# Performance work log

Measured on AMD Instinct MI355X. Metric: run time of the kernel, lower is better.

## Reference

```python
import jax, jax.numpy as jnp
import numpy as np
import math

TILE_SIZE = 32
N_HEADS = 16
FACTOR = 5.0
MASK_VALUE = -1e9


def setup_inputs() -> dict:
    key = jax.random.key(0)
    ks = jax.random.split(key, 8)
    B, S, D = 2, 2048, 1024
    w = 0.02  # weight scale so attention logits stay in a sane range
    return {
        "query": jax.random.normal(ks[0], (B, S, D), jnp.float32),
        "key": jax.random.normal(ks[1], (B, S, D), jnp.float32),
        "value": jax.random.normal(ks[2], (B, S, D), jnp.float32),
        "mask": jnp.zeros((1, 1, S, S), jnp.float32),
        "Wq": jax.random.normal(ks[3], (D, D), jnp.float32) * w,
        "bq": jnp.zeros((D,), jnp.float32),
        "Wk": jax.random.normal(ks[4], (D, D), jnp.float32) * w,
        "bk": jnp.zeros((D,), jnp.float32),
        "Wv": jax.random.normal(ks[5], (D, D), jnp.float32) * w,
        "bv": jnp.zeros((D,), jnp.float32),
        "Wo": jax.random.normal(ks[6], (D, D), jnp.float32) * w,
        "bo": jnp.zeros((D,), jnp.float32),
        "q_valid_len": 2000,
        "k_valid_len": 1900,
    }


def _pad_to_multiple(x, multiple):
    L = x.shape[1]
    p = (-L) % multiple  # static
    if p:
        x = jnp.pad(x, ((0, 0), (0, p), (0, 0)))
    return x, L


def _split_heads(x, H):
    B, L, D = x.shape
    return x.reshape(B, L, H, D // H).transpose(0, 2, 1, 3)  # [B,H,L,hd]


def _forward(query, key, value, mask, Wq, bq, Wk, bk, Wv, bv, Wo, bo,
             q_valid_len, k_valid_len):
    B, Sq, D = query.shape
    H = N_HEADS
    hd = D // H
    q = query @ Wq.T + bq
    k = key @ Wk.T + bk
    v = value @ Wv.T + bv
    q, q_len_pad = _pad_to_multiple(q, TILE_SIZE)
    k, _ = _pad_to_multiple(k, TILE_SIZE)
    v, _ = _pad_to_multiple(v, TILE_SIZE)
    qh, kh, vh = _split_heads(q, H), _split_heads(k, H), _split_heads(v, H)
    Lq, Lk = qh.shape[2], kh.shape[2]

    # key padding mask [1,1,1,Lk]
    kpm = ((jnp.arange(Lk) >= k_valid_len).astype(jnp.float32) * MASK_VALUE)
    attn_mask = mask + kpm.reshape(1, 1, 1, Lk)

    # manual scaled-dot attention with bf16 cast of scores (stable softmax path)
    scores = jnp.einsum('bhqd,bhkd->bhqk', qh, kh) / math.sqrt(hd)
    scores = scores.astype(jnp.bfloat16) + attn_mask.astype(jnp.bfloat16)
    probs = jax.nn.softmax(scores, axis=-1).astype(vh.dtype)
    context = jnp.einsum('bhqk,bhkd->bhqd', probs, vh)

    # ProbSparse top-u query-selection mask (note: original passes q_len_pad,
    # the pre-padding length, as valid_length)
    u = max(1, int(FACTOR * math.log(max(2, q_valid_len))))
    q_norm = jnp.sum(qh * qh, axis=-1)  # [B,H,Lq]
    if q_len_pad < Lq:
        q_norm = jnp.where(jnp.arange(Lq) < q_len_pad, q_norm, MASK_VALUE)
    _, topk_idx = jax.lax.top_k(q_norm, u)  # [B,H,u]
    # scatter ones at top-u positions (indices unique -> one-hot sum == set)
    ps_mask = jnp.sum(jax.nn.one_hot(topk_idx, Lq, dtype=jnp.float32), axis=2)
    context = context * ps_mask[..., None]

    # merge heads, strip padding, output projection (dropout p=0 / eval)
    context = context.transpose(0, 2, 1, 3).reshape(B, Lq, D)[:, :Sq, :]
    return context @ Wo.T + bo


def reference(query, key, value, mask, Wq, bq, Wk, bk, Wv, bv, Wo, bo,
              q_valid_len, k_valid_len):
    return _forward(query, key, value, mask, Wq, bq, Wk, bk, Wv, bv, Wo, bo,
                    q_valid_len, k_valid_len)
```

## Files before the change

kernel.cpp:

```cpp
#include <hip/hip_runtime.h>

typedef unsigned short u16;
typedef __bf16 bf16x8 __attribute__((ext_vector_type(8)));
typedef float f32x4 __attribute__((ext_vector_type(4)));

__device__ __forceinline__ u16 f2bf(float f){
  unsigned int x = __float_as_uint(f);
  unsigned int r = (x + 0x7FFFu + ((x >> 16) & 1u)) >> 16;
  return (u16)r;
}
__device__ __forceinline__ float bf2f(u16 u){
  return __uint_as_float(((unsigned int)u) << 16);
}
__device__ __forceinline__ int compute_u(int qvlv){
  int mm = qvlv > 2 ? qvlv : 2;
  int u = (int)(5.0 * log((double)mm));
  if (u < 1) u = 1;
  if (u > 64) u = 64;
  return u;
}
__device__ __forceinline__ void gload_lds16(const void* g, void* l){
  __builtin_amdgcn_global_load_lds(
      (const __attribute__((address_space(1))) void*)g,
      (__attribute__((address_space(3))) void*)l, 16, 0, 0);
}

__global__ void expand_kernel(const float* __restrict__ xq, const float* __restrict__ xk,
                              const float* __restrict__ xv,
                              const float* __restrict__ wq, const float* __restrict__ wk,
                              const float* __restrict__ wv,
                              u16* __restrict__ X1, u16* __restrict__ X2,
                              u16* __restrict__ W1, u16* __restrict__ W2)
{
  size_t g = (size_t)blockIdx.x * 256 + threadIdx.x;
  const float* src; u16 *d1, *d2;
  if (g < 3145728ull) {
    int p = (int)(g >> 20);
    size_t e = (g & 1048575ull) * 4;
    src = (p == 0 ? xq : (p == 1 ? xk : xv)) + e;
    size_t o = (size_t)p * 4194304ull + e;
    d1 = X1 + o; d2 = X2 + o;
  } else {
    size_t wg = g - 3145728ull;
    int p = (int)(wg >> 18);
    size_t e = (wg & 262143ull) * 4;
    src = (p == 0 ? wq : (p == 1 ? wk : wv)) + e;
    size_t o = (size_t)p * 1048576ull + e;
    d1 = W1 + o; d2 = W2 + o;
  }
  float4 x = *reinterpret_cast<const float4*>(src);
  float xs[4] = {x.x, x.y, x.z, x.w};
  u16 h1[4], h2[4];
#pragma unroll
  for (int i = 0; i < 4; ++i){
    float v = xs[i];
    u16 a = f2bf(v);  float r1 = v - bf2f(a);
    h1[i] = a; h2[i] = f2bf(r1);
  }
  *reinterpret_cast<ushort4*>(d1) = make_ushort4(h1[0], h1[1], h1[2], h1[3]);
  *reinterpret_cast<ushort4*>(d2) = make_ushort4(h2[0], h2[1], h2[2], h2[3]);
}

__global__ void wot_kernel(const float* __restrict__ Wo, float* __restrict__ WoT){
  __shared__ float tile[32][33];
  int tx = threadIdx.x, ty = threadIdx.y;
  int bx = blockIdx.x * 32, by = blockIdx.y * 32;
#pragma unroll
  for (int r = 0; r < 4; ++r)
    tile[ty + r*8][tx] = Wo[(size_t)(by + ty + r*8) * 1024 + bx + tx];
  __syncthreads();
#pragma unroll
  for (int r = 0; r < 4; ++r)
    WoT[(size_t)(bx + ty + r*8) * 1024 + by + tx] = tile[tx][ty + r*8];
}

__global__ __launch_bounds__(512, 1) void gemm_proj(
    const u16* __restrict__ X1, const u16* __restrict__ X2,
    const u16* __restrict__ W1, const u16* __restrict__ W2,
    const float* __restrict__ bq, const float* __restrict__ bk, const float* __restrict__ bv,
    float* __restrict__ PROJ)
{
  int z = blockIdx.z;
  int orig = blockIdx.x + blockIdx.y * 8;
  int wgid = (orig & 7) * 16 + (orig >> 3);
  int bx = wgid & 7, by = wgid >> 3;

  const u16* Xa0 = X1 + (size_t)z * 4194304;
  const u16* Xa1 = X2 + (size_t)z * 4194304;
  const u16* Wb0 = W1 + (size_t)z * 1048576;
  const u16* Wb1 = W2 + (size_t)z * 1048576;
  const float* bias = (z == 0) ? bq : (z == 1 ? bk : bv);
  float* C = PROJ + (size_t)z * 4194304;

  __shared__ __align__(16) u16 T[2 * 24576];
  u16* SET0 = T;
  u16* SET1 = T + 24576;

  int t = threadIdx.x;
  int wave = t >> 6, lane = t & 63;
  int wm = wave >> 1, wn = wave & 1;
  int lr = lane & 15, lk = lane >> 4;
  int rowA = by * 256, rowB = bx * 128;
  f32x4 acc[4][4] = {};
  bf16x8 afA[4], afB[4], bgA[4], bgB[4];

#define STAGEA(dstbase, G)                                                    \
  {                                                                           \
    _Pragma("unroll")                                                         \
    for (int i = 0; i < 2; ++i){                                              \
      int p = i * 512 + t;                                                    \
      int r = p >> 2;                                                         \
      int c = (p & 3) ^ ((r >> 1) & 3);                                       \
      gload_lds16(G + (size_t)(rowA + r) * 1024 + pk + c * 8,                 \
                  (dstbase) + p * 8);                                         \
    }                                                                         \
  }
#define STAGEB(dstbase, G)                                                    \
  {                                                                           \
    int p = t;                                                                \
    int r = p >> 2;                                                           \
    int c = (p & 3) ^ ((r >> 1) & 3);                                         \
    gload_lds16(G + (size_t)(rowB + r) * 1024 + pk + c * 8,                   \
                (dstbase) + p * 8);                                           \
  }
#define STAGE_SET(S)                                                          \
  {                                                                           \
    STAGEA((S), Xa0); STAGEA((S) + 8192, Xa1);                                \
    STAGEB((S) + 16384, Wb0); STAGEB((S) + 20480, Wb1);                       \
  }
#define LOADA(dst, tile)                                                      \
  {                                                                           \
    _Pragma("unroll")                                                         \
    for (int m = 0; m < 4; ++m){                                              \
      int r = wm * 64 + m * 16 + lr;                                          \
      dst[m] = *reinterpret_cast<const bf16x8*>(                              \
          &(tile)[r * 32 + ((lk ^ ((r >> 1) & 3)) << 3)]);                    \
    }                                                                         \
  }
#define LOADB(dst, tile)                                                      \
  {                                                                           \
    _Pragma("unroll")                                                         \
    for (int n = 0; n < 4; ++n){                                              \
      int r = wn * 64 + n * 16 + lr;                                          \
      dst[n] = *reinterpret_cast<const bf16x8*>(                              \
          &(tile)[r * 32 + ((lk ^ ((r >> 1) & 3)) << 3)]);                    \
    }                                                                         \
  }
#define GRPX(A_, B_)                                                          \
  {                                                                           \
    __builtin_amdgcn_s_setprio(1);                                            \
    _Pragma("unroll")                                                         \
    for (int m = 0; m < 4; ++m)                                               \
      _Pragma("unroll")                                                       \
      for (int n = 0; n < 4; ++n)                                             \
        acc[m][n] = __builtin_amdgcn_mfma_f32_16x16x32_bf16(A_[m], B_[n],     \
                                                            acc[m][n], 0,0,0);\
    __builtin_amdgcn_s_setprio(0);                                            \
  }

  {
    int pk = 0;
    STAGE_SET(SET0);
  }
  __syncthreads();

  for (int kt = 0; kt < 32; ++kt){
    u16* CUR = (kt & 1) ? SET1 : SET0;
    u16* NXT = (kt & 1) ? SET0 : SET1;
    if (kt < 31){
      int pk = (kt + 1) * 32;
      STAGE_SET(NXT);
    }
    __builtin_amdgcn_sched_barrier(0);
    u16* A0t = CUR;          u16* A1t = CUR + 8192;
    u16* B0t = CUR + 16384;  u16* B1t = CUR + 20480;
    LOADA(afA, A0t); LOADB(bgA, B0t);
    LOADB(bgB, B1t); GRPX(afA, bgA);
    LOADA(afB, A1t); GRPX(afA, bgB);
                     GRPX(afB, bgA);
    __syncthreads();
  }
#undef STAGEA
#undef STAGEB
#undef STAGE_SET
#undef LOADA
#undef LOADB
#undef GRPX

  if (z == 0){
#pragma unroll
    for (int m = 0; m < 4; ++m){
      int row0 = by * 256 + wm * 64 + m * 16 + lk * 4;
#pragma unroll
      for (int n = 0; n < 4; ++n){
        int col = bx * 128 + wn * 64 + n * 16 + lr;
        float bb = bias[col];
#pragma unroll
        for (int j = 0; j < 4; ++j)
          C[(size_t)(row0 + j) * 1024 + col] = acc[m][n][j] + bb;
      }
    }
  } else if (z == 1){
    u16* KS = (u16*)C;
#pragma unroll
    for (int m = 0; m < 4; ++m){
      int r0 = by * 256 + wm * 64 + m * 16 + lk * 4;
      int b = r0 >> 11, kb = r0 & 2047;
#pragma unroll
      for (int n = 0; n < 4; ++n){
        int c = bx * 128 + wn * 64 + n * 16 + lr;
        float bb = bias[c];
        int h = c >> 6, d = c & 63;
#pragma unroll
        for (int j = 0; j < 4; ++j){
          float v = acc[m][n][j] + bb;
          u16 hi = f2bf(v);
          u16 lo = f2bf(v - bf2f(hi));
          size_t base = ((size_t)(b * 16 + h) * 2048 + (size_t)(kb + j)) * 128;
          KS[base + d] = hi;
          KS[base + 64 + d] = lo;
        }
      }
    }
  } else {
    u16* VT = (u16*)C;
#pragma unroll
    for (int m = 0; m < 4; ++m){
      int r0 = by * 256 + wm * 64 + m * 16 + lk * 4;
      int b = r0 >> 11, kb = r0 & 2047;
#pragma unroll
      for (int n = 0; n < 4; ++n){
        int c = bx * 128 + wn * 64 + n * 16 + lr;
        float bb = bias[c];
        int h = c >> 6, d = c & 63;
        u16 hi[4], lo[4];
#pragma unroll
        for (int j = 0; j < 4; ++j){
          float v = acc[m][n][j] + bb;
          hi[j] = f2bf(v);
          lo[j] = f2bf(v - bf2f(hi[j]));
        }
        size_t base = ((size_t)(b * 16 + h) * 128) * 2048 + (size_t)kb;
        *reinterpret_cast<ushort4*>(&VT[base + (size_t)d * 2048]) =
            make_ushort4(hi[0], hi[1], hi[2], hi[3]);
        *reinterpret_cast<ushort4*>(&VT[base + (size_t)(64 + d) * 2048]) =
            make_ushort4(lo[0], lo[1], lo[2], lo[3]);
      }
    }
  }
}

__global__ __launch_bounds__(256) void qnorm_kernel(const float* __restrict__ PROJ,
                                                    float* __restrict__ qn,
                                                    unsigned int* __restrict__ hmask){
  int t = threadIdx.x;
  int gid = blockIdx.x * 256 + t;
  if (gid < 4096) hmask[gid] = 0;
  int h = t >> 4, q4 = t & 15;
#pragma unroll
  for (int it = 0; it < 8; ++it){
    int tok = blockIdx.x * 8 + it;
    const float* row = PROJ + (size_t)tok * 1024;
    float4 x = *reinterpret_cast<const float4*>(&row[h * 64 + q4 * 4]);
    float s = x.x*x.x + x.y*x.y + x.z*x.z + x.w*x.w;
    s += __shfl_xor(s, 1);
    s += __shfl_xor(s, 2);
    s += __shfl_xor(s, 4);
    s += __shfl_xor(s, 8);
    if (q4 == 0){
      int b = tok >> 11, l = tok & 2047;
      qn[(size_t)(b * 16 + h) * 2048 + l] = s;
    }
  }
}

__global__ __launch_bounds__(512) void topk_kernel(
    const float* __restrict__ qn, int* __restrict__ topk,
    unsigned char* __restrict__ seli, unsigned int* __restrict__ hmask,
    const int* __restrict__ qvlp){
  int bh = blockIdx.x; int b = bh >> 4, h = bh & 15;
  int u = compute_u(qvlp[0]);
  int t = threadIdx.x;
  float4 v4 = *reinterpret_cast<const float4*>(qn + (size_t)bh * 2048 + t * 4);
  float v[4] = {v4.x, v4.y, v4.z, v4.w};
  __shared__ float swv[8];
  __shared__ int swi[8];
  __shared__ int sidx;
  int lane = t & 63, w = t >> 6;
  for (int it = 0; it < u; ++it){
    float bv = v[0]; int bi = t * 4;
#pragma unroll
    for (int j = 1; j < 4; ++j){
      if (v[j] > bv){ bv = v[j]; bi = t * 4 + j; }
    }
#pragma unroll
    for (int off = 1; off < 64; off <<= 1){
      float ov = __shfl_xor(bv, off);
      int   oi = __shfl_xor(bi, off);
      if (ov > bv || (ov == bv && oi < bi)){ bv = ov; bi = oi; }
    }
    if (lane == 0){ swv[w] = bv; swi[w] = bi; }
    __syncthreads();
    if (t == 0){
      float fv = swv[0]; int fi = swi[0];
#pragma unroll
      for (int k = 1; k < 8; ++k){
        if (swv[k] > fv || (swv[k] == fv && swi[k] < fi)){ fv = swv[k]; fi = swi[k]; }
      }
      sidx = fi;
      topk[bh * 64 + it] = fi;
      seli[(size_t)bh * 2048 + fi] = (unsigned char)it;
      atomicOr(&hmask[b * 2048 + fi], 1u << h);
    }
    __syncthreads();
    int idx = sidx;
    if ((idx >> 2) == t) v[idx & 3] = -3.4e38f;
  }
}

__global__ void qs_gather(const float* __restrict__ PROJ, const int* __restrict__ topk,
                          u16* __restrict__ QS, const int* __restrict__ qvlp){
  int bh = blockIdx.x; int b = bh >> 4, h = bh & 15;
  int u = compute_u(qvlp[0]);
  __shared__ int idx[64];
  int t = threadIdx.x;
  if (t < 64) idx[t] = (t < u) ? topk[bh * 64 + t] : 0;
  __syncthreads();
  for (int e = t; e < 64 * 64; e += 256){
    int i = e >> 6, d = e & 63;
    float v = 0.f;
    if (i < u) v = PROJ[(size_t)(b * 2048 + idx[i]) * 1024 + h * 64 + d];
    u16 hi = f2bf(v);
    u16 lo = f2bf(v - bf2f(hi));
    QS[(size_t)bh * 8192 + i * 128 + d] = hi;
    QS[(size_t)bh * 8192 + i * 128 + 64 + d] = lo;
  }
}

__global__ __launch_bounds__(256) void scores_mfma(
    const u16* __restrict__ QS, const u16* __restrict__ KS,
    const int* __restrict__ topk, const float* __restrict__ maskp,
    u16* __restrict__ sc, const int* __restrict__ qvlp, const int* __restrict__ kvlp)
{
  int bh = blockIdx.y;
  int kvlv = kvlp[0]; if (kvlv > 2048) kvlv = 2048; if (kvlv < 0) kvlv = 0;
  int u = compute_u(qvlp[0]);
  int k0 = blockIdx.x * 128;
  if (k0 >= kvlv) return;
  int t = threadIdx.x, wave = t >> 6, lane = t & 63;
  int lr = lane & 15, lk = lane >> 4;
  __shared__ int idx_l[64];
  if (t < 64) idx_l[t] = (t < u) ? topk[bh * 64 + t] : 0;
  __syncthreads();
  const u16* Qb = QS + (size_t)bh * 8192;
  const u16* Kb = KS + (size_t)bh * 2048 * 128;
  bf16x8 ah[2], al[2];
#pragma unroll
  for (int ks = 0; ks < 2; ++ks){
    const u16* qrow = &Qb[(wave * 16 + lr) * 128];
    ah[ks] = *reinterpret_cast<const bf16x8*>(&qrow[ks * 32 + lk * 8]);
    al[ks] = *reinterpret_cast<const bf16x8*>(&qrow[64 + ks * 32 + lk * 8]);
  }
  f32x4 acc[8] = {};
#pragma unroll
  for (int n = 0; n < 8; ++n){
    const u16* krow = &Kb[(size_t)(k0 + n * 16 + lr) * 128];
    bf16x8 bh0 = *reinterpret_cast<const bf16x8*>(&krow[lk * 8]);
    bf16x8 bh1 = *reinterpret_cast<const bf16x8*>(&krow[32 + lk * 8]);
    bf16x8 bl0 = *reinterpret_cast<const bf16x8*>(&krow[64 + lk * 8]);
    bf16x8 bl1 = *reinterpret_cast<const bf16x8*>(&krow[96 + lk * 8]);
    acc[n] = __builtin_amdgcn_mfma_f32_16x16x32_bf16(ah[0], bh0, acc[n], 0, 0, 0);
    acc[n] = __builtin_amdgcn_mfma_f32_16x16x32_bf16(ah[0], bl0, acc[n], 0, 0, 0);
    acc[n] = __builtin_amdgcn_mfma_f32_16x16x32_bf16(al[0], bh0, acc[n], 0, 0, 0);
    acc[n] = __builtin_amdgcn_mfma_f32_16x16x32_bf16(al[0], bl0, acc[n], 0, 0, 0);
    acc[n] = __builtin_amdgcn_mfma_f32_16x16x32_bf16(ah[1], bh1, acc[n], 0, 0, 0);
    acc[n] = __builtin_amdgcn_mfma_f32_16x16x32_bf16(ah[1], bl1, acc[n], 0, 0, 0);
    acc[n] = __builtin_amdgcn_mfma_f32_16x16x32_bf16(al[1], bh1, acc[n], 0, 0, 0);
    acc[n] = __builtin_amdgcn_mfma_f32_16x16x32_bf16(al[1], bl1, acc[n], 0, 0, 0);
  }
#pragma unroll
  for (int n = 0; n < 8; ++n){
    int k = k0 + n * 16 + lr;
    if (k >= kvlv) continue;
#pragma unroll
    for (int j = 0; j < 4; ++j){
      int i = wave * 16 + lk * 4 + j;
      if (i >= u) continue;
      float s = acc[n][j] * 0.125f;
      u16 xb = f2bf(s);
      u16 mb = f2bf(maskp[(size_t)idx_l[i] * 2048 + k]);
      u16 xm = f2bf(bf2f(xb) + bf2f(mb));
      sc[(size_t)(bh * 64 + i) * 2048 + k] = xm;
    }
  }
}

__global__ void softmax_kernel(u16* __restrict__ sc, const int* __restrict__ qvlp,
                               const int* __restrict__ kvlp){
  int bh = blockIdx.y, i = blockIdx.x;
  int u = compute_u(qvlp[0]);
  if (i >= u) return;
  int kvlv = kvlp[0]; if (kvlv > 2048) kvlv = 2048; if (kvlv < 0) kvlv = 0;
  u16* row = sc + (size_t)(bh * 64 + i) * 2048;
  int t = threadIdx.x;
  float x[8];
  float lm = -3.4e38f;
#pragma unroll
  for (int j = 0; j < 8; ++j){
    int k = t + j * 256;
    x[j] = (k < kvlv) ? bf2f(row[k]) : -3.4e38f;
    lm = fmaxf(lm, x[j]);
  }
  __shared__ float red[256];
  red[t] = lm; __syncthreads();
  for (int s = 128; s > 0; s >>= 1){ if (t < s) red[t] = fmaxf(red[t], red[t+s]); __syncthreads(); }
  float m = red[0];
  __syncthreads();
  float e[8]; float ls = 0.f;
#pragma unroll
  for (int j = 0; j < 8; ++j){
    int k = t + j * 256;
    if (k < kvlv){
      u16 ub = f2bf(x[j] - m);
      u16 eb = f2bf(expf(bf2f(ub)));
      e[j] = bf2f(eb);
      ls += e[j];
    } else e[j] = 0.f;
  }
  red[t] = ls; __syncthreads();
  for (int s = 128; s > 0; s >>= 1){ if (t < s) red[t] += red[t+s]; __syncthreads(); }
  float S = red[0];
  float Sb = bf2f(f2bf(S));
#pragma unroll
  for (int j = 0; j < 8; ++j){
    int k = t + j * 256;
    if (k < 2048) row[k] = (k < kvlv) ? f2bf(e[j] / Sb) : (u16)0;
  }
}

__global__ void pv_mfma(const u16* __restrict__ probs, const u16* __restrict__ VT,
                        float* __restrict__ part, const int* __restrict__ kvlp)
{
  int bh = blockIdx.y; int b = bh >> 4, h = bh & 15;
  int kvlv = kvlp[0]; if (kvlv > 2048) kvlv = 2048; if (kvlv < 0) kvlv = 0;
  int kc = blockIdx.x;
  int k0 = kc * 128;
  if (k0 >= kvlv) return;
  int t = threadIdx.x, w = t >> 6, lane = t & 63;
  int lr = lane & 15, lk = lane >> 4;
  const u16* Pb = probs + (size_t)bh * 64 * 2048;
  const u16* Vb = VT + (size_t)(b * 16 + h) * 128 * 2048;
  f32x4 acc[4] = {};
#pragma unroll
  for (int ks = 0; ks < 4; ++ks){
    int kk = k0 + ks * 32 + lk * 8;
    bf16x8 A0 = *reinterpret_cast<const bf16x8*>(Pb + (size_t)(lr     ) * 2048 + kk);
    bf16x8 A1 = *reinterpret_cast<const bf16x8*>(Pb + (size_t)(lr + 16) * 2048 + kk);
    bf16x8 A2 = *reinterpret_cast<const bf16x8*>(Pb + (size_t)(lr + 32) * 2048 + kk);
    bf16x8 A3 = *reinterpret_cast<const bf16x8*>(Pb + (size_t)(lr + 48) * 2048 + kk);
    bf16x8 Bh = *reinterpret_cast<const bf16x8*>(Vb + (size_t)(w * 16 + lr     ) * 2048 + kk);
    bf16x8 Bl = *reinterpret_cast<const bf16x8*>(Vb + (size_t)(w * 16 + lr + 64) * 2048 + kk);
    acc[0] = __builtin_amdgcn_mfma_f32_16x16x32_bf16(A0, Bh, acc[0], 0, 0, 0);
    acc[1] = __builtin_amdgcn_mfma_f32_16x16x32_bf16(A1, Bh, acc[1], 0, 0, 0);
    acc[2] = __builtin_amdgcn_mfma_f32_16x16x32_bf16(A2, Bh, acc[2], 0, 0, 0);
    acc[3] = __builtin_amdgcn_mfma_f32_16x16x32_bf16(A3, Bh, acc[3], 0, 0, 0);
    acc[0] = __builtin_amdgcn_mfma_f32_16x16x32_bf16(A0, Bl, acc[0], 0, 0, 0);
    acc[1] = __builtin_amdgcn_mfma_f32_16x16x32_bf16(A1, Bl, acc[1], 0, 0, 0);
    acc[2] = __builtin_amdgcn_mfma_f32_16x16x32_bf16(A2, Bl, acc[2], 0, 0, 0);
    acc[3] = __builtin_amdgcn_mfma_f32_16x16x32_bf16(A3, Bl, acc[3], 0, 0, 0);
  }
  float* pc = part + (size_t)(kc * 32 + bh) * 64 * 64;
#pragma unroll
  for (int m = 0; m < 4; ++m){
    int row = m * 16 + lk * 4;
#pragma unroll
    for (int j = 0; j < 4; ++j)
      pc[(size_t)(row + j) * 64 + w * 16 + lr] = acc[m][j];
  }
}

__global__ void pv_reduce(const float* __restrict__ part, float* __restrict__ ctx,
                          const int* __restrict__ qvlp, const int* __restrict__ kvlp){
  int bh = blockIdx.y, r = blockIdx.x;
  int u = compute_u(qvlp[0]);
  if (r >= u) return;
  int kvlv = kvlp[0]; if (kvlv > 2048) kvlv = 2048; if (kvlv < 0) kvlv = 0;
  int kcmax = (kvlv + 127) / 128;
  int d = threadIdx.x;
  float s = 0.f;
  for (int kc = 0; kc < kcmax; ++kc)
    s += part[(size_t)((kc * 32 + bh) * 64 + r) * 64 + d];
  ctx[(size_t)(bh * 64 + r) * 64 + d] = s;
}

__global__ void outproj_kernel(const float* __restrict__ ctx, const float* __restrict__ WoT,
                               const float* __restrict__ bo, const unsigned int* __restrict__ hmask,
                               const unsigned char* __restrict__ seli, float* __restrict__ out){
  int row = blockIdx.x;
  int b = row >> 11, l = row & 2047;
  int t = threadIdx.x;
  float acc[4];
#pragma unroll
  for (int r = 0; r < 4; ++r) acc[r] = bo[t + r * 256];
  unsigned int m = hmask[row];
  __shared__ float clds[64];
  while (m){
    int h = __ffs(m) - 1; m &= (m - 1);
    int i = (int)seli[(size_t)(b * 16 + h) * 2048 + l];
    __syncthreads();
    if (t < 64) clds[t] = ctx[(size_t)((b * 16 + h) * 64 + i) * 64 + t];
    __syncthreads();
    for (int j = 0; j < 64; ++j){
      float c = clds[j];
      const float* wrow = &WoT[(size_t)(h * 64 + j) * 1024];
#pragma unroll
      for (int r = 0; r < 4; ++r) acc[r] += c * wrow[t + r * 256];
    }
  }
  float* orow = out + (size_t)row * 1024;
#pragma unroll
  for (int r = 0; r < 4; ++r) orow[t + r * 256] = acc[r];
}

__global__ void fail_fill(float* o, int n){
  int i = blockIdx.x * 256 + threadIdx.x;
  if (i < n) o[i] = 12345.0f;
}

extern "C" void kernel_launch(void* const* d_in, const int* in_sizes, int n_in,
                              void* d_out, int out_size, void* d_ws, size_t ws_size,
                              hipStream_t stream)
{
  const float* query = (const float*)d_in[0];
  const float* key   = (const float*)d_in[1];
  const float* value = (const float*)d_in[2];
  const float* maskp = (const float*)d_in[3];
  const float* Wq = (const float*)d_in[4];
  const float* bq = (const float*)d_in[5];
  const float* Wk = (const float*)d_in[6];
  const float* bk = (const float*)d_in[7];
  const float* Wv = (const float*)d_in[8];
  const float* bv = (const float*)d_in[9];
  const float* Wo = (const float*)d_in[10];
  const float* bo = (const float*)d_in[11];
  const int* qvl = (const int*)d_in[12];
  const int* kvl = (const int*)d_in[13];
  float* out = (float*)d_out;

  char* ws = (char*)d_ws;
  size_t off = 0;
  auto alloc = [&](size_t bytes) -> void* {
    void* p = ws + off;
    off = (off + bytes + 255) & ~(size_t)255;
    return p;
  };
  u16* X1 = (u16*)alloc(3ull * 4194304 * 2);
  u16* X2 = (u16*)alloc(3ull * 4194304 * 2);
  u16* W1 = (u16*)alloc(3ull * 1048576 * 2);
  u16* W2 = (u16*)alloc(3ull * 1048576 * 2);
  float* PROJ = (float*)alloc(3ull * 4194304 * 4);
  float* WOT  = (float*)alloc(4194304ull);
  float* QN   = (float*)alloc(2ull * 16 * 2048 * 4);
  int*   TOPK = (int*)alloc(2ull * 16 * 64 * 4);
  unsigned char* SELI = (unsigned char*)alloc(2ull * 16 * 2048);
  unsigned int* HMASK = (unsigned int*)alloc(2ull * 2048 * 4);
  u16*   SC   = (u16*)alloc(2048ull * 2048 * 2);
  float* CTX  = (float*)alloc(2048ull * 64 * 4);
  u16*   QS   = (u16*)alloc(32ull * 64 * 128 * 2);

  u16* KS = (u16*)(PROJ + 1ull * 4194304);
  u16* VT = (u16*)(PROJ + 2ull * 4194304);
  float* PART = (float*)X1;

  if (ws_size < off){
    fail_fill<<<(out_size + 255) / 256, 256, 0, stream>>>(out, out_size);
    return;
  }

  expand_kernel<<<15360, 256, 0, stream>>>(query, key, value, Wq, Wk, Wv,
                                           X1, X2, W1, W2);
  wot_kernel<<<dim3(32, 32), dim3(32, 8), 0, stream>>>(Wo, WOT);
  gemm_proj<<<dim3(8, 16, 3), 512, 0, stream>>>(X1, X2, W1, W2, bq, bk, bv, PROJ);
  qnorm_kernel<<<512, 256, 0, stream>>>(PROJ, QN, HMASK);
  topk_kernel<<<32, 512, 0, stream>>>(QN, TOPK, SELI, HMASK, qvl);
  qs_gather<<<32, 256, 0, stream>>>(PROJ, TOPK, QS, qvl);
  scores_mfma<<<dim3(16, 32), 256, 0, stream>>>(QS, KS, TOPK, maskp, SC, qvl, kvl);
  softmax_kernel<<<dim3(64, 32), 256, 0, stream>>>(SC, qvl, kvl);
  pv_mfma<<<dim3(16, 32), 256, 0, stream>>>(SC, VT, PART, kvl);
  pv_reduce<<<dim3(64, 32), 64, 0, stream>>>(PART, CTX, qvl, kvl);
  outproj_kernel<<<4096, 256, 0, stream>>>(CTX, WOT, bo, HMASK, SELI, out);
}
```

Measured before the change: 259.3 us.

## Fuse small kernels: WoT into expand, qnorm into GEMM epilogue, topk+gather, reduce into outproj

Merges the Wo transpose and hmask clearing into the expand kernel. Computes per-head query norms in the Q-projection GEMM epilogue using shuffles instead of rereading PROJ. Replaces the block-wide top-k with a single-wavefront register top-k fused with the QS gather, and folds the partial-sum reduction into the output projection. The goal is to cut kernel launches and global round trips. The cost is a serial single-wave top-k and redundant partial reductions for each selected row in outproj.

```diff
diff --git a/kernel.cpp b/kernel.cpp
--- a/kernel.cpp
+++ b/kernel.cpp
@@ -30,9 +30,27 @@
                               const float* __restrict__ wq, const float* __restrict__ wk,
                               const float* __restrict__ wv,
                               u16* __restrict__ X1, u16* __restrict__ X2,
-                              u16* __restrict__ W1, u16* __restrict__ W2)
+                              u16* __restrict__ W1, u16* __restrict__ W2,
+                              const float* __restrict__ Wo, float* __restrict__ WoT,
+                              unsigned int* __restrict__ hmask)
 {
-  size_t g = (size_t)blockIdx.x * 256 + threadIdx.x;
+  __shared__ float tile[32][33];
+  int t = threadIdx.x;
+  if (blockIdx.x >= 15360){
+    int bid = blockIdx.x - 15360;
+    int bx = (bid & 31) * 32, by = (bid >> 5) * 32;
+    int tx = t & 31, ty = t >> 5;
+#pragma unroll
+    for (int r = 0; r < 4; ++r)
+      tile[ty + r*8][tx] = Wo[(size_t)(by + ty + r*8) * 1024 + bx + tx];
+    __syncthreads();
+#pragma unroll
+    for (int r = 0; r < 4; ++r)
+      WoT[(size_t)(bx + ty + r*8) * 1024 + by + tx] = tile[tx][ty + r*8];
+    return;
+  }
+  size_t g = (size_t)blockIdx.x * 256 + t;
+  if (g < 4096) hmask[g] = 0;
   const float* src; u16 *d1, *d2;
   if (g < 3145728ull) {
     int p = (int)(g >> 20);
@@ -61,24 +79,11 @@
   *reinterpret_cast<ushort4*>(d2) = make_ushort4(h2[0], h2[1], h2[2], h2[3]);
 }
 
-__global__ void wot_kernel(const float* __restrict__ Wo, float* __restrict__ WoT){
-  __shared__ float tile[32][33];
-  int tx = threadIdx.x, ty = threadIdx.y;
-  int bx = blockIdx.x * 32, by = blockIdx.y * 32;
-#pragma unroll
-  for (int r = 0; r < 4; ++r)
-    tile[ty + r*8][tx] = Wo[(size_t)(by + ty + r*8) * 1024 + bx + tx];
-  __syncthreads();
-#pragma unroll
-  for (int r = 0; r < 4; ++r)
-    WoT[(size_t)(bx + ty + r*8) * 1024 + by + tx] = tile[tx][ty + r*8];
-}
-
 __global__ __launch_bounds__(512, 1) void gemm_proj(
     const u16* __restrict__ X1, const u16* __restrict__ X2,
     const u16* __restrict__ W1, const u16* __restrict__ W2,
     const float* __restrict__ bq, const float* __restrict__ bk, const float* __restrict__ bv,
-    float* __restrict__ PROJ)
+    float* __restrict__ PROJ, float* __restrict__ qn)
 {
   int z = blockIdx.z;
   int orig = blockIdx.x + blockIdx.y * 8;
@@ -188,6 +193,7 @@
 #undef GRPX
 
   if (z == 0){
+    float sq[4][4] = {};
 #pragma unroll
     for (int m = 0; m < 4; ++m){
       int row0 = by * 256 + wm * 64 + m * 16 + lk * 4;
@@ -196,8 +202,27 @@
         int col = bx * 128 + wn * 64 + n * 16 + lr;
         float bb = bias[col];
 #pragma unroll
-        for (int j = 0; j < 4; ++j)
-          C[(size_t)(row0 + j) * 1024 + col] = acc[m][n][j] + bb;
+        for (int j = 0; j < 4; ++j){
+          float v = acc[m][n][j] + bb;
+          C[(size_t)(row0 + j) * 1024 + col] = v;
+          sq[m][j] += v * v;
+        }
+      }
+    }
+    int hh = bx * 2 + wn;
+#pragma unroll
+    for (int m = 0; m < 4; ++m){
+#pragma unroll
+      for (int j = 0; j < 4; ++j){
+        float s = sq[m][j];
+        s += __shfl_xor(s, 1);
+        s += __shfl_xor(s, 2);
+        s += __shfl_xor(s, 4);
+        s += __shfl_xor(s, 8);
+        if (lr == 0){
+          int row = by * 256 + wm * 64 + m * 16 + lk * 4 + j;
+          qn[(size_t)((row >> 11) * 16 + hh) * 2048 + (row & 2047)] = s;
+        }
       }
     }
   } else if (z == 1){
@@ -250,86 +275,48 @@
   }
 }
 
-__global__ __launch_bounds__(256) void qnorm_kernel(const float* __restrict__ PROJ,
-                                                    float* __restrict__ qn,
-                                                    unsigned int* __restrict__ hmask){
-  int t = threadIdx.x;
-  int gid = blockIdx.x * 256 + t;
-  if (gid < 4096) hmask[gid] = 0;
-  int h = t >> 4, q4 = t & 15;
-#pragma unroll
-  for (int it = 0; it < 8; ++it){
-    int tok = blockIdx.x * 8 + it;
-    const float* row = PROJ + (size_t)tok * 1024;
-    float4 x = *reinterpret_cast<const float4*>(&row[h * 64 + q4 * 4]);
-    float s = x.x*x.x + x.y*x.y + x.z*x.z + x.w*x.w;
-    s += __shfl_xor(s, 1);
-    s += __shfl_xor(s, 2);
-    s += __shfl_xor(s, 4);
-    s += __shfl_xor(s, 8);
-    if (q4 == 0){
-      int b = tok >> 11, l = tok & 2047;
-      qn[(size_t)(b * 16 + h) * 2048 + l] = s;
-    }
-  }
-}
-
-__global__ __launch_bounds__(512) void topk_kernel(
+__global__ __launch_bounds__(256) void topk_kernel(
     const float* __restrict__ qn, int* __restrict__ topk,
     unsigned char* __restrict__ seli, unsigned int* __restrict__ hmask,
+    const float* __restrict__ PROJ, u16* __restrict__ QS,
     const int* __restrict__ qvlp){
   int bh = blockIdx.x; int b = bh >> 4, h = bh & 15;
   int u = compute_u(qvlp[0]);
   int t = threadIdx.x;
-  float4 v4 = *reinterpret_cast<const float4*>(qn + (size_t)bh * 2048 + t * 4);
-  float v[4] = {v4.x, v4.y, v4.z, v4.w};
-  __shared__ float swv[8];
-  __shared__ int swi[8];
-  __shared__ int sidx;
-  int lane = t & 63, w = t >> 6;
-  for (int it = 0; it < u; ++it){
-    float bv = v[0]; int bi = t * 4;
-#pragma unroll
-    for (int j = 1; j < 4; ++j){
-      if (v[j] > bv){ bv = v[j]; bi = t * 4 + j; }
-    }
-#pragma unroll
-    for (int off = 1; off < 64; off <<= 1){
-      float ov = __shfl_xor(bv, off);
-      int   oi = __shfl_xor(bi, off);
-      if (ov > bv || (ov == bv && oi < bi)){ bv = ov; bi = oi; }
-    }
-    if (lane == 0){ swv[w] = bv; swi[w] = bi; }
-    __syncthreads();
-    if (t == 0){
-      float fv = swv[0]; int fi = swi[0];
-#pragma unroll
-      for (int k = 1; k < 8; ++k){
-        if (swv[k] > fv || (swv[k] == fv && swi[k] < fi)){ fv = swv[k]; fi = swi[k]; }
-      }
-      sidx = fi;
-      topk[bh * 64 + it] = fi;
-      seli[(size_t)bh * 2048 + fi] = (unsigned char)it;
-      atomicOr(&hmask[b * 2048 + fi], 1u << h);
-    }
-    __syncthreads();
-    int idx = sidx;
-    if ((idx >> 2) == t) v[idx & 3] = -3.4e38f;
-  }
-}
-
-__global__ void qs_gather(const float* __restrict__ PROJ, const int* __restrict__ topk,
-                          u16* __restrict__ QS, const int* __restrict__ qvlp){
-  int bh = blockIdx.x; int b = bh >> 4, h = bh & 15;
-  int u = compute_u(qvlp[0]);
-  __shared__ int idx[64];
-  int t = threadIdx.x;
-  if (t < 64) idx[t] = (t < u) ? topk[bh * 64 + t] : 0;
+  __shared__ int sidx_l[64];
+  if (t < 64){
+    int lane = t;
+    float v[32];
+#pragma unroll
+    for (int j = 0; j < 32; ++j) v[j] = qn[(size_t)bh * 2048 + j * 64 + lane];
+    for (int it = 0; it < u; ++it){
+      float bv = v[0]; int bi = lane;
+#pragma unroll
+      for (int j = 1; j < 32; ++j){
+        if (v[j] > bv){ bv = v[j]; bi = j * 64 + lane; }
+      }
+#pragma unroll
+      for (int off = 1; off < 64; off <<= 1){
+        float ov = __shfl_xor(bv, off);
+        int   oi = __shfl_xor(bi, off);
+        if (ov > bv || (ov == bv && oi < bi)){ bv = ov; bi = oi; }
+      }
+      if (lane == 0){
+        topk[bh * 64 + it] = bi;
+        seli[(size_t)bh * 2048 + bi] = (unsigned char)it;
+        atomicOr(&hmask[b * 2048 + bi], 1u << h);
+        sidx_l[it] = bi;
+      }
+#pragma unroll
+      for (int j = 0; j < 32; ++j)
+        if (j * 64 + lane == bi) v[j] = -3.4e38f;
+    }
+  }
   __syncthreads();
   for (int e = t; e < 64 * 64; e += 256){
     int i = e >> 6, d = e & 63;
     float v = 0.f;
-    if (i < u) v = PROJ[(size_t)(b * 2048 + idx[i]) * 1024 + h * 64 + d];
+    if (i < u) v = PROJ[(size_t)(b * 2048 + sidx_l[i]) * 1024 + h * 64 + d];
     u16 hi = f2bf(v);
     u16 lo = f2bf(v - bf2f(hi));
     QS[(size_t)bh * 8192 + i * 128 + d] = hi;
@@ -479,26 +466,15 @@
   }
 }
 
-__global__ void pv_reduce(const float* __restrict__ part, float* __restrict__ ctx,
-                          const int* __restrict__ qvlp, const int* __restrict__ kvlp){
-  int bh = blockIdx.y, r = blockIdx.x;
-  int u = compute_u(qvlp[0]);
-  if (r >= u) return;
-  int kvlv = kvlp[0]; if (kvlv > 2048) kvlv = 2048; if (kvlv < 0) kvlv = 0;
-  int kcmax = (kvlv + 127) / 128;
-  int d = threadIdx.x;
-  float s = 0.f;
-  for (int kc = 0; kc < kcmax; ++kc)
-    s += part[(size_t)((kc * 32 + bh) * 64 + r) * 64 + d];
-  ctx[(size_t)(bh * 64 + r) * 64 + d] = s;
-}
-
-__global__ void outproj_kernel(const float* __restrict__ ctx, const float* __restrict__ WoT,
+__global__ void outproj_kernel(const float* __restrict__ part, const float* __restrict__ WoT,
                                const float* __restrict__ bo, const unsigned int* __restrict__ hmask,
-                               const unsigned char* __restrict__ seli, float* __restrict__ out){
+                               const unsigned char* __restrict__ seli, float* __restrict__ out,
+                               const int* __restrict__ kvlp){
   int row = blockIdx.x;
   int b = row >> 11, l = row & 2047;
   int t = threadIdx.x;
+  int kvlv = kvlp[0]; if (kvlv > 2048) kvlv = 2048; if (kvlv < 0) kvlv = 0;
+  int kcmax = (kvlv + 127) / 128;
   float acc[4];
 #pragma unroll
   for (int r = 0; r < 4; ++r) acc[r] = bo[t + r * 256];
@@ -506,9 +482,15 @@
   __shared__ float clds[64];
   while (m){
     int h = __ffs(m) - 1; m &= (m - 1);
-    int i = (int)seli[(size_t)(b * 16 + h) * 2048 + l];
+    int bh = b * 16 + h;
+    int i = (int)seli[(size_t)bh * 2048 + l];
     __syncthreads();
-    if (t < 64) clds[t] = ctx[(size_t)((b * 16 + h) * 64 + i) * 64 + t];
+    if (t < 64){
+      float s = 0.f;
+      for (int kc = 0; kc < kcmax; ++kc)
+        s += part[(size_t)((kc * 32 + bh) * 64 + i) * 64 + t];
+      clds[t] = s;
+    }
     __syncthreads();
     for (int j = 0; j < 64; ++j){
       float c = clds[j];
@@ -565,7 +547,6 @@
   unsigned char* SELI = (unsigned char*)alloc(2ull * 16 * 2048);
   unsigned int* HMASK = (unsigned int*)alloc(2ull * 2048 * 4);
   u16*   SC   = (u16*)alloc(2048ull * 2048 * 2);
-  float* CTX  = (float*)alloc(2048ull * 64 * 4);
   u16*   QS   = (u16*)alloc(32ull * 64 * 128 * 2);
 
   u16* KS = (u16*)(PROJ + 1ull * 4194304);
@@ -577,16 +558,12 @@
     return;
   }
 
-  expand_kernel<<<15360, 256, 0, stream>>>(query, key, value, Wq, Wk, Wv,
-                                           X1, X2, W1, W2);
-  wot_kernel<<<dim3(32, 32), dim3(32, 8), 0, stream>>>(Wo, WOT);
-  gemm_proj<<<dim3(8, 16, 3), 512, 0, stream>>>(X1, X2, W1, W2, bq, bk, bv, PROJ);
-  qnorm_kernel<<<512, 256, 0, stream>>>(PROJ, QN, HMASK);
-  topk_kernel<<<32, 512, 0, stream>>>(QN, TOPK, SELI, HMASK, qvl);
-  qs_gather<<<32, 256, 0, stream>>>(PROJ, TOPK, QS, qvl);
+  expand_kernel<<<16384, 256, 0, stream>>>(query, key, value, Wq, Wk, Wv,
+                                           X1, X2, W1, W2, Wo, WOT, HMASK);
+  gemm_proj<<<dim3(8, 16, 3), 512, 0, stream>>>(X1, X2, W1, W2, bq, bk, bv, PROJ, QN);
+  topk_kernel<<<32, 256, 0, stream>>>(QN, TOPK, SELI, HMASK, PROJ, QS, qvl);
   scores_mfma<<<dim3(16, 32), 256, 0, stream>>>(QS, KS, TOPK, maskp, SC, qvl, kvl);
   softmax_kernel<<<dim3(64, 32), 256, 0, stream>>>(SC, qvl, kvl);
   pv_mfma<<<dim3(16, 32), 256, 0, stream>>>(SC, VT, PART, kvl);
-  pv_reduce<<<dim3(64, 32), 64, 0, stream>>>(PART, CTX, qvl, kvl);
-  outproj_kernel<<<4096, 256, 0, stream>>>(CTX, WOT, bo, HMASK, SELI, out);
-}
+  outproj_kernel<<<4096, 256, 0, stream>>>(PART, WOT, bo, HMASK, SELI, out, kvl);
+}
```

New measurement: 252.4 us. 1.03x faster.
